# Kernel tuning notes

Hardware: AMD Instinct MI355X
Metric: run time of the kernel (lower is better)

Reference implementation:

```python
import jax, jax.numpy as jnp
import numpy as np

N, FDIM, HDIM, STEPS = 8192, 512, 1024, 50
STRESS, QNOISE = 0.0, 0.1


def setup_inputs() -> dict:
    key = jax.random.key(0)
    ks = jax.random.split(key, 20)
    s = 0.02
    d = {
        "real_antigen": jax.random.normal(ks[0], (N, FDIM), jnp.float32),
        "steps": STEPS,
        # quantum gene projection (self-loop graph -> per-node linear)
        "Wq": jax.random.normal(ks[1], (FDIM, HDIM), jnp.float32) * s,
        "bq": jnp.zeros((HDIM,), jnp.float32),
        # denoise_0: Linear(h,h) ReLU Linear(h,f)
        "W01": jax.random.normal(ks[2], (HDIM, HDIM), jnp.float32) * s,
        "b01": jnp.zeros((HDIM,), jnp.float32),
        "W02": jax.random.normal(ks[3], (HDIM, FDIM), jnp.float32) * s,
        "b02": jnp.zeros((FDIM,), jnp.float32),
        # denoise_1: Linear(h,h) Tanh Linear(h,f)
        "W11": jax.random.normal(ks[4], (HDIM, HDIM), jnp.float32) * s,
        "b11": jnp.zeros((HDIM,), jnp.float32),
        "W12": jax.random.normal(ks[5], (HDIM, FDIM), jnp.float32) * s,
        "b12": jnp.zeros((FDIM,), jnp.float32),
        # interference_net: Linear(2f,h) GELU Linear(h,f)
        "Wi1": jax.random.normal(ks[6], (2 * FDIM, HDIM), jnp.float32) * s,
        "bi1": jnp.zeros((HDIM,), jnp.float32),
        "Wi2": jax.random.normal(ks[7], (HDIM, FDIM), jnp.float32) * s,
        "bi2": jnp.zeros((FDIM,), jnp.float32),
        # quantum state scalars
        "alpha_amp": jnp.asarray(np.cos(0.6), jnp.float32),
        "beta_amp": jnp.asarray(np.sin(0.6), jnp.float32),
        "phase_cos": jnp.asarray(np.cos(0.3), jnp.float32),
    }
    return d


def reference(real_antigen, steps, Wq, bq, W01, b01, W02, b02, W11, b11,
              W12, b12, Wi1, bi1, Wi2, bi2, alpha_amp, beta_amp, phase_cos):
    sched = jnp.linspace(1e-4, 0.02, 100, dtype=jnp.float32)
    decoherence_rate = jnp.float32(0.1 + STRESS * 0.5)
    decay = jnp.exp(-decoherence_rate)
    # quantum probabilities (fixed amplitudes during the rollout)
    a2, b2 = alpha_amp ** 2, beta_amp ** 2
    p0 = a2 / (a2 + b2)
    p1 = b2 / (a2 + b2)
    sp0, sp1 = jnp.sqrt(p0), jnp.sqrt(p1)
    base_key = jax.random.key(1)
    x0 = jax.random.normal(jax.random.fold_in(base_key, 10_000), real_antigen.shape, jnp.float32)

    def step(carry, t):
        x, coh = carry
        qf = jax.nn.relu(x @ Wq + bq)                           # [N, H]
        d0 = jax.nn.relu(qf @ W01 + b01) @ W02 + b02            # [N, F]
        d1 = jnp.tanh(qf @ W11 + b11) @ W12 + b12               # [N, F]
        inter_in = jnp.concatenate([d0, d1], axis=-1)           # [N, 2F]
        interf = jax.nn.gelu(inter_in @ Wi1 + bi1, approximate=False) @ Wi2 + bi2
        qi = 2.0 * jnp.sqrt(p0 * p1) * phase_cos * coh          # scalar interference
        denoised = sp0 * d0 + sp1 * d1 + qi * interf
        alpha = jnp.maximum(1.0 - sched[t], 1e-8)
        alpha_prev = jnp.where(t > 0, 1.0 - sched[jnp.maximum(t - 1, 0)], 1.0)
        sqrt_1ma = jnp.sqrt(jnp.maximum(1.0 - alpha, 1e-8))
        x_new = (x - (1.0 - alpha) / sqrt_1ma * denoised) / jnp.sqrt(alpha)
        sigma = jnp.sqrt(jnp.maximum((1.0 - alpha_prev) / (1.0 - alpha) * (1.0 - alpha / alpha_prev), 0.0))
        noise = jax.random.normal(jax.random.fold_in(base_key, t), x.shape, jnp.float32)
        x_new = jnp.where(t > 0, x_new + (sigma + QNOISE * jnp.abs(qi)) * noise, x_new)
        return (x_new, coh * decay), None

    ts = jnp.arange(int(steps) - 1, -1, -1, dtype=jnp.int32)
    (x, _), _ = jax.lax.scan(step, (x0, jnp.float32(1.0)), ts)
    # quantum measurement: collapse to |0> with probability p0
    u = jax.random.uniform(jax.random.fold_in(base_key, 99_999), (), jnp.float32)
    dream = jnp.where(u < p0, 0.7 * x + 0.3 * real_antigen, x)
    return dream
```

## Files before the change

### kernel.cpp

```cpp
#include <hip/hip_runtime.h>
#include <stdint.h>
#include <math.h>


typedef __bf16 bf16x8 __attribute__((ext_vector_type(8)));
typedef float floatx4 __attribute__((ext_vector_type(4)));

__host__ __device__ inline void tf2x32(uint32_t k0, uint32_t k1,
                                       uint32_t x0, uint32_t x1,
                                       uint32_t& o0, uint32_t& o1) {
  uint32_t ks2 = k0 ^ k1 ^ 0x1BD11BDAu;
#define TF_R(r) { x0 += x1; x1 = (x1 << (r)) | (x1 >> (32 - (r))); x1 ^= x0; }
  x0 += k0; x1 += k1;
  TF_R(13) TF_R(15) TF_R(26) TF_R(6)
  x0 += k1;  x1 += ks2 + 1u;
  TF_R(17) TF_R(29) TF_R(16) TF_R(24)
  x0 += ks2; x1 += k0 + 2u;
  TF_R(13) TF_R(15) TF_R(26) TF_R(6)
  x0 += k0;  x1 += k1 + 3u;
  TF_R(17) TF_R(29) TF_R(16) TF_R(24)
  x0 += k1;  x1 += ks2 + 4u;
  TF_R(13) TF_R(15) TF_R(26) TF_R(6)
  x0 += ks2; x1 += k0 + 5u;
#undef TF_R
  o0 = x0; o1 = x1;
}

__device__ inline float erfinv_f32(float x) {
  float w = -log1pf(-x * x);
  float p;
  if (w < 5.0f) {
    w = w - 2.5f;
    p = 2.81022636e-08f;
    p = fmaf(p, w, 3.43273939e-07f);
    p = fmaf(p, w, -3.5233877e-06f);
    p = fmaf(p, w, -4.39150654e-06f);
    p = fmaf(p, w, 0.00021858087f);
    p = fmaf(p, w, -0.00125372503f);
    p = fmaf(p, w, -0.00417768164f);
    p = fmaf(p, w, 0.246640727f);
    p = fmaf(p, w, 1.50140941f);
  } else {
    w = sqrtf(w) - 3.0f;
    p = -0.000200214257f;
    p = fmaf(p, w, 0.000100950558f);
    p = fmaf(p, w, 0.00134934322f);
    p = fmaf(p, w, -0.00367342844f);
    p = fmaf(p, w, 0.00573950773f);
    p = fmaf(p, w, -0.0076224613f);
    p = fmaf(p, w, 0.00943887047f);
    p = fmaf(p, w, 1.00167406f);
    p = fmaf(p, w, 2.83297682f);
  }
  return p * x;
}

__device__ inline float tf_normal(uint32_t k0, uint32_t k1, uint32_t i) {
  uint32_t o0, o1;
  tf2x32(k0, k1, 0u, i, o0, o1);
  uint32_t bits = o0 ^ o1;
  float f = __uint_as_float(0x3F800000u | (bits >> 9)) - 1.0f;
  float u = f * 2.0f + (-0.99999994f);
  u = fmaxf(-0.99999994f, u);
  return 1.41421356f * erfinv_f32(u);
}

__device__ inline unsigned short f2bf(float f) {
  uint32_t u = __float_as_uint(f);
  u += 0x7FFFu + ((u >> 16) & 1u);
  return (unsigned short)(u >> 16);
}
__device__ inline float bf2f(unsigned short h) {
  return __uint_as_float(((uint32_t)h) << 16);
}

__global__ __launch_bounds__(256)
void transpose_bf16_kernel(const float* __restrict__ W,
                           unsigned short* __restrict__ Wt, int K, int N) {
  __shared__ float tile[32][33];
  int kb = blockIdx.x * 32, nb = blockIdx.y * 32;
  int tx = threadIdx.x & 31, ty = threadIdx.x >> 5;
#pragma unroll
  for (int i = 0; i < 32; i += 8)
    tile[ty + i][tx] = W[(size_t)(kb + ty + i) * N + nb + tx];
  __syncthreads();
#pragma unroll
  for (int i = 0; i < 32; i += 8)
    Wt[(size_t)(nb + ty + i) * K + kb + tx] = f2bf(tile[tx][ty + i]);
}

__device__ __forceinline__ void gemm_core_db(
    const unsigned short* __restrict__ A0, const unsigned short* __restrict__ A1,
    int lda0, int lda1, int K0, int Ktot,
    const unsigned short* __restrict__ Bt,
    int row0, int col0,
    unsigned short (*As)[128 * 32], unsigned short (*Bs)[128 * 32],
    floatx4 (&acc)[2][4]) {
  const int tid = threadIdx.x;
  const int wave = tid >> 6, lane = tid & 63;
  const int wr = wave >> 1, wc = wave & 1;
  const int srow = tid >> 2;
  const int sgr = (tid & 3) * 8;
  const int fm = lane & 15, quad = lane >> 4;

  auto issue = [&](int kt, int buf) {
    const int k0 = kt * 32;
    const unsigned short* Ap; int kOff, lda;
    if (k0 < K0) { Ap = A0; kOff = k0; lda = lda0; }
    else         { Ap = A1; kOff = k0 - K0; lda = lda1; }
    __builtin_amdgcn_global_load_lds(
        (const __attribute__((address_space(1))) uint32_t*)
            (Ap + (size_t)(row0 + srow) * lda + kOff + sgr),
        (__attribute__((address_space(3))) uint32_t*)(&As[buf][srow * 32 + sgr]),
        16, 0, 0);
    __builtin_amdgcn_global_load_lds(
        (const __attribute__((address_space(1))) uint32_t*)
            (Bt + (size_t)(col0 + srow) * Ktot + k0 + sgr),
        (__attribute__((address_space(3))) uint32_t*)(&Bs[buf][srow * 32 + sgr]),
        16, 0, 0);
  };

  const int nk = Ktot >> 5;
  issue(0, 0);
  for (int k = 0; k < nk; k++) {
    const int cur = k & 1;
    if (k + 1 < nk) {
      issue(k + 1, cur ^ 1);
      asm volatile("s_waitcnt vmcnt(2)\ns_barrier" ::: "memory");
    } else {
      asm volatile("s_waitcnt vmcnt(0)\ns_barrier" ::: "memory");
    }
    bf16x8 a[2], b[4];
#pragma unroll
    for (int tm = 0; tm < 2; tm++)
      a[tm] = *(const bf16x8*)(&As[cur][(wr * 32 + tm * 16 + fm) * 32 + quad * 8]);
#pragma unroll
    for (int tn = 0; tn < 4; tn++)
      b[tn] = *(const bf16x8*)(&Bs[cur][(wc * 64 + tn * 16 + fm) * 32 + quad * 8]);
#pragma unroll
    for (int tm = 0; tm < 2; tm++)
#pragma unroll
      for (int tn = 0; tn < 4; tn++)
        acc[tm][tn] = __builtin_amdgcn_mfma_f32_16x16x32_bf16(a[tm], b[tn],
                                                              acc[tm][tn], 0, 0, 0);
    asm volatile("s_barrier" ::: "memory");
  }
}

__device__ __forceinline__ void swizzled_block(int& row0, int& col0) {
  int id = blockIdx.x + gridDim.x * blockIdx.y;
  row0 = (id & 63) << 7;
  col0 = (id >> 6) << 7;
}

template<int ACT>
__global__ __launch_bounds__(512, 4)
void mfma_gemm(const unsigned short* __restrict__ A0,
               const unsigned short* __restrict__ A1,
               int lda0, int lda1, int K0, int Ktot,
               const unsigned short* __restrict__ Bt,
               const float* __restrict__ bias0,
               const float* __restrict__ bias1, int nsplit,
               unsigned short* __restrict__ C0,
               unsigned short* __restrict__ C1, int ldc) {
  __shared__ unsigned short As[2][128 * 32];
  __shared__ unsigned short Bs[2][128 * 32];
  int row0, col0;
  swizzled_block(row0, col0);
  floatx4 acc[2][4];
#pragma unroll
  for (int tm = 0; tm < 2; tm++)
#pragma unroll
    for (int tn = 0; tn < 4; tn++) acc[tm][tn] = (floatx4){0.f, 0.f, 0.f, 0.f};
  gemm_core_db(A0, A1, lda0, lda1, K0, Ktot, Bt, row0, col0, As, Bs, acc);

  const int lane = threadIdx.x & 63, wave = threadIdx.x >> 6;
  const int wr = wave >> 1, wc = wave & 1;
  const int fm = lane & 15, quad = lane >> 4;
  const bool side = (ACT == 4) && (col0 >= nsplit);
  const float* bias = side ? bias1 : bias0;
  unsigned short* C = side ? C1 : C0;
  const int cbase = col0 - (side ? nsplit : 0);
#pragma unroll
  for (int tn = 0; tn < 4; tn++) {
    int col = cbase + wc * 64 + tn * 16 + fm;
    float bv = bias[col];
#pragma unroll
    for (int tm = 0; tm < 2; tm++) {
      int rbase = row0 + wr * 32 + tm * 16 + quad * 4;
#pragma unroll
      for (int r = 0; r < 4; r++) {
        float val = acc[tm][tn][r] + bv;
        if (ACT == 1) val = fmaxf(val, 0.0f);
        if (ACT == 2) val = tanhf(val);
        if (ACT == 3) val = 0.5f * val * (1.0f + erff(val * 0.70710678118654752f));
        if (ACT == 4) val = side ? tanhf(val) : fmaxf(val, 0.0f);
        C[(size_t)(rbase + r) * ldc + col] = f2bf(val);
      }
    }
  }
}

__global__ __launch_bounds__(512, 4)
void mfma_gemm_pair(const unsigned short* __restrict__ Aa,
                    const unsigned short* __restrict__ Ab,
                    const unsigned short* __restrict__ Bta,
                    const unsigned short* __restrict__ Btb,
                    const float* __restrict__ biasa,
                    const float* __restrict__ biasb,
                    unsigned short* __restrict__ Ca,
                    unsigned short* __restrict__ Cb,
                    int Ktot, int ldc) {
  __shared__ unsigned short As[2][128 * 32];
  __shared__ unsigned short Bs[2][128 * 32];
  const int z = blockIdx.z;
  const unsigned short* A = z ? Ab : Aa;
  const unsigned short* Bt = z ? Btb : Bta;
  const float* bias = z ? biasb : biasa;
  unsigned short* C = z ? Cb : Ca;
  int row0, col0;
  swizzled_block(row0, col0);
  floatx4 acc[2][4];
#pragma unroll
  for (int tm = 0; tm < 2; tm++)
#pragma unroll
    for (int tn = 0; tn < 4; tn++) acc[tm][tn] = (floatx4){0.f, 0.f, 0.f, 0.f};
  gemm_core_db(A, A, Ktot, Ktot, Ktot, Ktot, Bt, row0, col0, As, Bs, acc);

  const int lane = threadIdx.x & 63, wave = threadIdx.x >> 6;
  const int wr = wave >> 1, wc = wave & 1;
  const int fm = lane & 15, quad = lane >> 4;
#pragma unroll
  for (int tn = 0; tn < 4; tn++) {
    int col = col0 + wc * 64 + tn * 16 + fm;
    float bv = bias[col];
#pragma unroll
    for (int tm = 0; tm < 2; tm++) {
      int rbase = row0 + wr * 32 + tm * 16 + quad * 4;
#pragma unroll
      for (int r = 0; r < 4; r++)
        C[(size_t)(rbase + r) * ldc + col] = f2bf(acc[tm][tn][r] + bv);
    }
  }
}

template<int MH, int NH>
__device__ __forceinline__ void phase_mfma8(bf16x8 (&a)[4][2], bf16x8 (&b)[4][2],
                                            floatx4 (&acc)[8][4]) {
  asm volatile("s_waitcnt lgkmcnt(0)" ::: "memory");
  __builtin_amdgcn_sched_barrier(0);
  __builtin_amdgcn_s_setprio(1);
#pragma unroll
  for (int s = 0; s < 2; s++)
#pragma unroll
    for (int mm = 0; mm < 4; mm++)
#pragma unroll
      for (int nn = 0; nn < 2; nn++)
        acc[MH * 4 + mm][NH * 2 + nn] = __builtin_amdgcn_mfma_f32_16x16x32_bf16(
            a[mm][s], b[NH * 2 + nn][s], acc[MH * 4 + mm][NH * 2 + nn], 0, 0, 0);
  __builtin_amdgcn_s_setprio(0);
}

__global__ __launch_bounds__(512, 2)
void mfma_gemm2_8ph(const unsigned short* __restrict__ A,
                    const unsigned short* __restrict__ Bt,
                    const float* __restrict__ bias0,
                    const float* __restrict__ bias1,
                    unsigned short* __restrict__ C0,
                    unsigned short* __restrict__ C1) {
  constexpr int NKT = 16;
  __shared__ unsigned short As[2][256 * 64];
  __shared__ unsigned short Bs[2][256 * 64];
  const int tid = threadIdx.x;
  const int wave = tid >> 6, lane = tid & 63;
  const int wr = wave >> 2, wc = wave & 3;
  const int fm = lane & 15, quad = lane >> 4;
  const int id = blockIdx.x;
  const int nid = (id & 7) * 32 + (id >> 3);
  const int row0 = (nid & 31) << 8;
  const int col0 = (nid >> 5) << 8;

  auto stageA = [&](int tile, int buf, int h) {
    if (tile >= NKT) return;
    const int kk = tile << 6;
#pragma unroll
    for (int c = 0; c < 2; c++) {
      int g2 = c * 512 + tid;
      int sr = g2 >> 3, gc = g2 & 7;
      __builtin_amdgcn_global_load_lds(
          (const __attribute__((address_space(1))) uint32_t*)
              (A + (size_t)(row0 + h * 128 + sr) * 1024 + kk + ((gc ^ (sr & 7)) << 3)),
          (__attribute__((address_space(3))) uint32_t*)(&As[buf][h * 8192 + g2 * 8]),
          16, 0, 0);
    }
  };
  auto stageB = [&](int tile, int buf, int h) {
    if (tile >= NKT) return;
    const int kk = tile << 6;
#pragma unroll
    for (int c = 0; c < 2; c++) {
      int g2 = c * 512 + tid;
      int sr = g2 >> 3, gc = g2 & 7;
      __builtin_amdgcn_global_load_lds(
          (const __attribute__((address_space(1))) uint32_t*)
              (Bt + (size_t)(col0 + h * 128 + sr) * 1024 + kk + ((gc ^ (sr & 7)) << 3)),
          (__attribute__((address_space(3))) uint32_t*)(&Bs[buf][h * 8192 + g2 * 8]),
          16, 0, 0);
    }
  };

  const int aswz = (fm & 7) << 3;
  auto rdA = [&](int buf, int m, int s) {
    return *(const bf16x8*)(&As[buf][(wr * 128 + m * 16 + fm) * 64 +
                                     ((s * 32 + quad * 8) ^ aswz)]);
  };
  auto rdB = [&](int buf, int n, int s) {
    return *(const bf16x8*)(&Bs[buf][(wc * 64 + n * 16 + fm) * 64 +
                                     ((s * 32 + quad * 8) ^ aswz)]);
  };

  floatx4 acc[8][4];
#pragma unroll
  for (int m = 0; m < 8; m++)
#pragma unroll
    for (int n = 0; n < 4; n++) acc[m][n] = (floatx4){0.f, 0.f, 0.f, 0.f};

  stageA(0, 0, 0); stageA(0, 0, 1);
  stageB(0, 0, 0); stageB(0, 0, 1);
  stageB(1, 1, 0); stageB(1, 1, 1);
  asm volatile("s_waitcnt vmcnt(4)" ::: "memory");
  asm volatile("s_barrier" ::: "memory");

#pragma unroll 1
  for (int j = 0; j < 8; j++) {
    const int t1 = 2 * j + 1;
    bf16x8 a[4][2], b[4][2];
#pragma unroll
    for (int mm = 0; mm < 4; mm++) { a[mm][0] = rdA(0, mm, 0); a[mm][1] = rdA(0, mm, 1); }
#pragma unroll
    for (int nn = 0; nn < 2; nn++) { b[nn][0] = rdB(0, nn, 0); b[nn][1] = rdB(0, nn, 1); }
    stageA(t1, 1, 0);
    asm volatile("s_barrier" ::: "memory");
    phase_mfma8<0, 0>(a, b, acc);
    asm volatile("s_barrier" ::: "memory");
#pragma unroll
    for (int nn = 2; nn < 4; nn++) { b[nn][0] = rdB(0, nn, 0); b[nn][1] = rdB(0, nn, 1); }
    stageA(t1, 1, 1);
    asm volatile("s_barrier" ::: "memory");
    phase_mfma8<0, 1>(a, b, acc);
    asm volatile("s_barrier" ::: "memory");
#pragma unroll
    for (int mm = 0; mm < 4; mm++) { a[mm][0] = rdA(0, 4 + mm, 0); a[mm][1] = rdA(0, 4 + mm, 1); }
    stageB(t1 + 1, 0, 0);
    asm volatile("s_barrier" ::: "memory");
    phase_mfma8<1, 1>(a, b, acc);
    asm volatile("s_barrier" ::: "memory");
    stageB(t1 + 1, 0, 1);
    asm volatile("s_barrier" ::: "memory");
    phase_mfma8<1, 0>(a, b, acc);
    if (j == 7) asm volatile("s_waitcnt vmcnt(0)" ::: "memory");
    else        asm volatile("s_waitcnt vmcnt(4)" ::: "memory");
    asm volatile("s_barrier" ::: "memory");
#pragma unroll
    for (int mm = 0; mm < 4; mm++) { a[mm][0] = rdA(1, mm, 0); a[mm][1] = rdA(1, mm, 1); }
#pragma unroll
    for (int nn = 0; nn < 2; nn++) { b[nn][0] = rdB(1, nn, 0); b[nn][1] = rdB(1, nn, 1); }
    stageA(t1 + 1, 0, 0);
    asm volatile("s_barrier" ::: "memory");
    phase_mfma8<0, 0>(a, b, acc);
    asm volatile("s_barrier" ::: "memory");
#pragma unroll
    for (int nn = 2; nn < 4; nn++) { b[nn][0] = rdB(1, nn, 0); b[nn][1] = rdB(1, nn, 1); }
    stageA(t1 + 1, 0, 1);
    asm volatile("s_barrier" ::: "memory");
    phase_mfma8<0, 1>(a, b, acc);
    asm volatile("s_barrier" ::: "memory");
#pragma unroll
    for (int mm = 0; mm < 4; mm++) { a[mm][0] = rdA(1, 4 + mm, 0); a[mm][1] = rdA(1, 4 + mm, 1); }
    stageB(t1 + 2, 1, 0);
    asm volatile("s_barrier" ::: "memory");
    phase_mfma8<1, 1>(a, b, acc);
    asm volatile("s_barrier" ::: "memory");
    stageB(t1 + 2, 1, 1);
    asm volatile("s_barrier" ::: "memory");
    phase_mfma8<1, 0>(a, b, acc);
    asm volatile("s_waitcnt vmcnt(4)" ::: "memory");
    asm volatile("s_barrier" ::: "memory");
  }

  const bool side = (col0 >= 1024);
  const float* bias = side ? bias1 : bias0;
  unsigned short* C = side ? C1 : C0;
  const int cb = col0 - (side ? 1024 : 0);
#pragma unroll
  for (int n = 0; n < 4; n++) {
    int col = cb + wc * 64 + n * 16 + fm;
    float bv = bias[col];
#pragma unroll
    for (int m = 0; m < 8; m++) {
      int rbase = row0 + wr * 128 + m * 16 + quad * 4;
#pragma unroll
      for (int r = 0; r < 4; r++) {
        float val = acc[m][n][r] + bv;
        val = side ? tanhf(val) : fmaxf(val, 0.0f);
        C[(size_t)(rbase + r) * 1024 + col] = f2bf(val);
      }
    }
  }
}

__global__ __launch_bounds__(512, 4)
void mfma_gemm_update(const unsigned short* __restrict__ A,
                      const unsigned short* __restrict__ Bt,
                      const float* __restrict__ bias,
                      const unsigned short* __restrict__ d0,
                      const unsigned short* __restrict__ d1,
                      float* __restrict__ x,
                      unsigned short* __restrict__ xbf,
                      const float* __restrict__ a_amp,
                      const float* __restrict__ b_amp,
                      const float* __restrict__ ph,
                      float coh, float c1, float sqa, float sigma,
                      int add_noise, uint32_t k0, uint32_t k1) {
  __shared__ unsigned short As[2][64 * 32];
  __shared__ unsigned short Bs[2][128 * 32];
  const int tid = threadIdx.x;
  const int wave = tid >> 6, lane = tid & 63;
  const int wr = wave >> 2, wc = wave & 3;
  const int fm = lane & 15, quad = lane >> 4;
  const int id = blockIdx.x + gridDim.x * blockIdx.y;
  const int row0 = (id & 127) << 6;
  const int col0 = (id >> 7) << 7;
  const int sArow = (tid & 255) >> 2;
  const int sBrow = tid >> 2;
  const int sgr = (tid & 3) * 8;

  auto issue = [&](int kt, int buf) {
    const int kk = kt * 32;
    __builtin_amdgcn_global_load_lds(
        (const __attribute__((address_space(1))) uint32_t*)
            (A + (size_t)(row0 + sArow) * 1024 + kk + sgr),
        (__attribute__((address_space(3))) uint32_t*)(&As[buf][sArow * 32 + sgr]),
        16, 0, 0);
    __builtin_amdgcn_global_load_lds(
        (const __attribute__((address_space(1))) uint32_t*)
            (Bt + (size_t)(col0 + sBrow) * 1024 + kk + sgr),
        (__attribute__((address_space(3))) uint32_t*)(&Bs[buf][sBrow * 32 + sgr]),
        16, 0, 0);
  };

  floatx4 acc[2][2];
#pragma unroll
  for (int tm = 0; tm < 2; tm++)
#pragma unroll
    for (int tn = 0; tn < 2; tn++) acc[tm][tn] = (floatx4){0.f, 0.f, 0.f, 0.f};

  const int nk = 32;
  issue(0, 0);
  for (int k = 0; k < nk; k++) {
    const int cur = k & 1;
    if (k + 1 < nk) {
      issue(k + 1, cur ^ 1);
      asm volatile("s_waitcnt vmcnt(2)\ns_barrier" ::: "memory");
    } else {
      asm volatile("s_waitcnt vmcnt(0)\ns_barrier" ::: "memory");
    }
    bf16x8 a[2], b[2];
#pragma unroll
    for (int tm = 0; tm < 2; tm++)
      a[tm] = *(const bf16x8*)(&As[cur][(wr * 32 + tm * 16 + fm) * 32 + quad * 8]);
#pragma unroll
    for (int tn = 0; tn < 2; tn++)
      b[tn] = *(const bf16x8*)(&Bs[cur][(wc * 32 + tn * 16 + fm) * 32 + quad * 8]);
#pragma unroll
    for (int tm = 0; tm < 2; tm++)
#pragma unroll
      for (int tn = 0; tn < 2; tn++)
        acc[tm][tn] = __builtin_amdgcn_mfma_f32_16x16x32_bf16(a[tm], b[tn],
                                                              acc[tm][tn], 0, 0, 0);
    asm volatile("s_barrier" ::: "memory");
  }

  float aa = a_amp[0], bb = b_amp[0], pc = ph[0];
  float a2 = aa * aa, b2 = bb * bb, s = a2 + b2;
  float p0 = a2 / s, p1 = b2 / s;
  float sp0 = sqrtf(p0), sp1 = sqrtf(p1);
  float qi = 2.0f * sqrtf(p0 * p1) * pc * coh;
  float nscale = sigma + 0.1f * fabsf(qi);

#pragma unroll
  for (int tn = 0; tn < 2; tn++) {
    int col = col0 + wc * 32 + tn * 16 + fm;
    float bv = bias[col];
#pragma unroll
    for (int tm = 0; tm < 2; tm++) {
      int rbase = row0 + wr * 32 + tm * 16 + quad * 4;
#pragma unroll
      for (int r = 0; r < 4; r++) {
        int row = rbase + r;
        size_t i = (size_t)row * 512 + col;
        float itf = acc[tm][tn][r] + bv;
        float den = sp0 * bf2f(d0[i]) + sp1 * bf2f(d1[i]) + qi * itf;
        float xn = (x[i] - c1 * den) / sqa;
        if (add_noise) xn += nscale * tf_normal(k0, k1, (uint32_t)i);
        x[i] = xn;
        xbf[i] = f2bf(xn);
      }
    }
  }
}

__global__ void init_normal_kernel(float* __restrict__ x,
                                   unsigned short* __restrict__ xbf,
                                   uint32_t k0, uint32_t k1, int n) {
  int i = blockIdx.x * blockDim.x + threadIdx.x;
  if (i >= n) return;
  float v = tf_normal(k0, k1, (uint32_t)i);
  x[i] = v;
  xbf[i] = f2bf(v);
}

__global__ void final_kernel(const float* __restrict__ x,
                             const float* __restrict__ real,
                             float* __restrict__ out,
                             const float* __restrict__ a_amp,
                             const float* __restrict__ b_amp,
                             uint32_t k0, uint32_t k1, int n) {
  int i = blockIdx.x * blockDim.x + threadIdx.x;
  if (i >= n) return;
  float aa = a_amp[0], bb = b_amp[0];
  float a2 = aa * aa, b2 = bb * bb;
  float p0 = a2 / (a2 + b2);
  uint32_t o0, o1;
  tf2x32(k0, k1, 0u, 0u, o0, o1);
  uint32_t bits = o0 ^ o1;
  float u = __uint_as_float(0x3F800000u | (bits >> 9)) - 1.0f;
  float xv = x[i];
  out[i] = (u < p0) ? (0.7f * xv + 0.3f * real[i]) : xv;
}

extern "C" void kernel_launch(void* const* d_in, const int* in_sizes, int n_in,
                              void* d_out, int out_size, void* d_ws,
                              size_t ws_size, hipStream_t stream) {
  const float* real = (const float*)d_in[0];
  const float* Wq  = (const float*)d_in[2];
  const float* bq  = (const float*)d_in[3];
  const float* W01 = (const float*)d_in[4];
  const float* b01 = (const float*)d_in[5];
  const float* W02 = (const float*)d_in[6];
  const float* b02 = (const float*)d_in[7];
  const float* W11 = (const float*)d_in[8];
  const float* b11 = (const float*)d_in[9];
  const float* W12 = (const float*)d_in[10];
  const float* b12 = (const float*)d_in[11];
  const float* Wi1 = (const float*)d_in[12];
  const float* bi1 = (const float*)d_in[13];
  const float* Wi2 = (const float*)d_in[14];
  const float* bi2 = (const float*)d_in[15];
  const float* a_amp = (const float*)d_in[16];
  const float* b_amp = (const float*)d_in[17];
  const float* ph    = (const float*)d_in[18];

  const int Nn = 8192, F = 512, H = 1024;
  const int nElem = Nn * F;
  const int NSPLIT_OFF = 1 << 30;

  char* ws = (char*)d_ws;
  float* x = (float*)ws;                                   ws += (size_t)nElem * 4;
  unsigned short* xbf = (unsigned short*)ws;               ws += (size_t)nElem * 2;
  unsigned short* qf  = (unsigned short*)ws;               ws += (size_t)Nn * H * 2;
  unsigned short* h0  = (unsigned short*)ws;               ws += (size_t)Nn * H * 2;
  unsigned short* h1  = (unsigned short*)ws;               ws += (size_t)Nn * H * 2;
  unsigned short* d0  = (unsigned short*)ws;               ws += (size_t)nElem * 2;
  unsigned short* d1  = (unsigned short*)ws;               ws += (size_t)nElem * 2;
  unsigned short* Wq_t  = (unsigned short*)ws;             ws += (size_t)F * H * 2;
  unsigned short* WA_t  = (unsigned short*)ws;             ws += (size_t)(2 * H) * H * 2;
  unsigned short* W02_t = (unsigned short*)ws;             ws += (size_t)H * F * 2;
  unsigned short* W12_t = (unsigned short*)ws;             ws += (size_t)H * F * 2;
  unsigned short* Wi1_t = (unsigned short*)ws;             ws += (size_t)(2 * F) * H * 2;
  unsigned short* Wi2_t = (unsigned short*)ws;             ws += (size_t)H * F * 2;

  dim3 tb(256);
  transpose_bf16_kernel<<<dim3(F / 32, H / 32), tb, 0, stream>>>(Wq, Wq_t, F, H);
  transpose_bf16_kernel<<<dim3(H / 32, H / 32), tb, 0, stream>>>(W01, WA_t, H, H);
  transpose_bf16_kernel<<<dim3(H / 32, H / 32), tb, 0, stream>>>(W11, WA_t + (size_t)H * H, H, H);
  transpose_bf16_kernel<<<dim3(H / 32, F / 32), tb, 0, stream>>>(W02, W02_t, H, F);
  transpose_bf16_kernel<<<dim3(H / 32, F / 32), tb, 0, stream>>>(W12, W12_t, H, F);
  transpose_bf16_kernel<<<dim3(2 * F / 32, H / 32), tb, 0, stream>>>(Wi1, Wi1_t, 2 * F, H);
  transpose_bf16_kernel<<<dim3(H / 32, F / 32), tb, 0, stream>>>(Wi2, Wi2_t, H, F);

  uint32_t kx0, kx1; tf2x32(0u, 1u, 0u, 10000u, kx0, kx1);
  init_normal_kernel<<<(nElem + 255) / 256, 256, 0, stream>>>(x, xbf, kx0, kx1, nElem);

  float sched[100];
  for (int i = 0; i < 100; i++)
    sched[i] = (float)(1e-4 + (0.02 - 1e-4) * (double)i / 99.0);
  const float decay = expf(-0.1f);
  float coh = 1.0f;

  dim3 blk(512);
  dim3 g1(H / 128, 64);
  dim3 g45(F / 128, 64, 2);
  dim3 g6(H / 128, 64);
  dim3 g7(F / 128, Nn / 64);

  for (int j = 0; j < 50; j++) {
    int t = 49 - j;
    mfma_gemm<1><<<g1, blk, 0, stream>>>(xbf, xbf, F, F, F, F, Wq_t,
                                         bq, nullptr, NSPLIT_OFF, qf, nullptr, H);
    mfma_gemm2_8ph<<<dim3(256), blk, 0, stream>>>(qf, WA_t, b01, b11, h0, h1);
    mfma_gemm_pair<<<g45, blk, 0, stream>>>(h0, h1, W02_t, W12_t, b02, b12,
                                            d0, d1, H, F);
    mfma_gemm<3><<<g6, blk, 0, stream>>>(d0, d1, F, F, F, 2 * F, Wi1_t,
                                         bi1, nullptr, NSPLIT_OFF, qf, nullptr, H);

    float schedt = sched[t];
    float alphaf = fmaxf(1.0f - schedt, 1e-8f);
    float one_m_alpha = 1.0f - alphaf;
    float sqrt_1ma = sqrtf(fmaxf(one_m_alpha, 1e-8f));
    float c1 = one_m_alpha / sqrt_1ma;
    float sqa = sqrtf(alphaf);
    float sigma = 0.0f;
    if (t > 0) {
      float ap = 1.0f - sched[t - 1];
      sigma = sqrtf(fmaxf((1.0f - ap) / one_m_alpha * (1.0f - alphaf / ap), 0.0f));
    }
    uint32_t kt0, kt1; tf2x32(0u, 1u, 0u, (uint32_t)t, kt0, kt1);
    mfma_gemm_update<<<g7, blk, 0, stream>>>(
        qf, Wi2_t, bi2, d0, d1, x, xbf, a_amp, b_amp, ph, coh, c1, sqa, sigma,
        (t > 0) ? 1 : 0, kt0, kt1);
    coh *= decay;
  }

  uint32_t ku0, ku1; tf2x32(0u, 1u, 0u, 99999u, ku0, ku1);
  final_kernel<<<(nElem + 255) / 256, 256, 0, stream>>>(
      x, real, (float*)d_out, a_amp, b_amp, ku0, ku1, nElem);
}
```

Baseline: 8.124 ms.

## Replace 128x128 double-buffered GEMMs with phased 128x256 swizzled-LDS kernel

```diff
diff --git a/kernel.cpp b/kernel.cpp
--- a/kernel.cpp
+++ b/kernel.cpp
@@ -89,161 +89,6 @@
     Wt[(size_t)(nb + ty + i) * K + kb + tx] = f2bf(tile[tx][ty + i]);
 }
 
-__device__ __forceinline__ void gemm_core_db(
-    const unsigned short* __restrict__ A0, const unsigned short* __restrict__ A1,
-    int lda0, int lda1, int K0, int Ktot,
-    const unsigned short* __restrict__ Bt,
-    int row0, int col0,
-    unsigned short (*As)[128 * 32], unsigned short (*Bs)[128 * 32],
-    floatx4 (&acc)[2][4]) {
-  const int tid = threadIdx.x;
-  const int wave = tid >> 6, lane = tid & 63;
-  const int wr = wave >> 1, wc = wave & 1;
-  const int srow = tid >> 2;
-  const int sgr = (tid & 3) * 8;
-  const int fm = lane & 15, quad = lane >> 4;
-
-  auto issue = [&](int kt, int buf) {
-    const int k0 = kt * 32;
-    const unsigned short* Ap; int kOff, lda;
-    if (k0 < K0) { Ap = A0; kOff = k0; lda = lda0; }
-    else         { Ap = A1; kOff = k0 - K0; lda = lda1; }
-    __builtin_amdgcn_global_load_lds(
-        (const __attribute__((address_space(1))) uint32_t*)
-            (Ap + (size_t)(row0 + srow) * lda + kOff + sgr),
-        (__attribute__((address_space(3))) uint32_t*)(&As[buf][srow * 32 + sgr]),
-        16, 0, 0);
-    __builtin_amdgcn_global_load_lds(
-        (const __attribute__((address_space(1))) uint32_t*)
-            (Bt + (size_t)(col0 + srow) * Ktot + k0 + sgr),
-        (__attribute__((address_space(3))) uint32_t*)(&Bs[buf][srow * 32 + sgr]),
-        16, 0, 0);
-  };
-
-  const int nk = Ktot >> 5;
-  issue(0, 0);
-  for (int k = 0; k < nk; k++) {
-    const int cur = k & 1;
-    if (k + 1 < nk) {
-      issue(k + 1, cur ^ 1);
-      asm volatile("s_waitcnt vmcnt(2)\ns_barrier" ::: "memory");
-    } else {
-      asm volatile("s_waitcnt vmcnt(0)\ns_barrier" ::: "memory");
-    }
-    bf16x8 a[2], b[4];
-#pragma unroll
-    for (int tm = 0; tm < 2; tm++)
-      a[tm] = *(const bf16x8*)(&As[cur][(wr * 32 + tm * 16 + fm) * 32 + quad * 8]);
-#pragma unroll
-    for (int tn = 0; tn < 4; tn++)
-      b[tn] = *(const bf16x8*)(&Bs[cur][(wc * 64 + tn * 16 + fm) * 32 + quad * 8]);
-#pragma unroll
-    for (int tm = 0; tm < 2; tm++)
-#pragma unroll
-      for (int tn = 0; tn < 4; tn++)
-        acc[tm][tn] = __builtin_amdgcn_mfma_f32_16x16x32_bf16(a[tm], b[tn],
-                                                              acc[tm][tn], 0, 0, 0);
-    asm volatile("s_barrier" ::: "memory");
-  }
-}
-
-__device__ __forceinline__ void swizzled_block(int& row0, int& col0) {
-  int id = blockIdx.x + gridDim.x * blockIdx.y;
-  row0 = (id & 63) << 7;
-  col0 = (id >> 6) << 7;
-}
-
-template<int ACT>
-__global__ __launch_bounds__(512, 4)
-void mfma_gemm(const unsigned short* __restrict__ A0,
-               const unsigned short* __restrict__ A1,
-               int lda0, int lda1, int K0, int Ktot,
-               const unsigned short* __restrict__ Bt,
-               const float* __restrict__ bias0,
-               const float* __restrict__ bias1, int nsplit,
-               unsigned short* __restrict__ C0,
-               unsigned short* __restrict__ C1, int ldc) {
-  __shared__ unsigned short As[2][128 * 32];
-  __shared__ unsigned short Bs[2][128 * 32];
-  int row0, col0;
-  swizzled_block(row0, col0);
-  floatx4 acc[2][4];
-#pragma unroll
-  for (int tm = 0; tm < 2; tm++)
-#pragma unroll
-    for (int tn = 0; tn < 4; tn++) acc[tm][tn] = (floatx4){0.f, 0.f, 0.f, 0.f};
-  gemm_core_db(A0, A1, lda0, lda1, K0, Ktot, Bt, row0, col0, As, Bs, acc);
-
-  const int lane = threadIdx.x & 63, wave = threadIdx.x >> 6;
-  const int wr = wave >> 1, wc = wave & 1;
-  const int fm = lane & 15, quad = lane >> 4;
-  const bool side = (ACT == 4) && (col0 >= nsplit);
-  const float* bias = side ? bias1 : bias0;
-  unsigned short* C = side ? C1 : C0;
-  const int cbase = col0 - (side ? nsplit : 0);
-#pragma unroll
-  for (int tn = 0; tn < 4; tn++) {
-    int col = cbase + wc * 64 + tn * 16 + fm;
-    float bv = bias[col];
-#pragma unroll
-    for (int tm = 0; tm < 2; tm++) {
-      int rbase = row0 + wr * 32 + tm * 16 + quad * 4;
-#pragma unroll
-      for (int r = 0; r < 4; r++) {
-        float val = acc[tm][tn][r] + bv;
-        if (ACT == 1) val = fmaxf(val, 0.0f);
-        if (ACT == 2) val = tanhf(val);
-        if (ACT == 3) val = 0.5f * val * (1.0f + erff(val * 0.70710678118654752f));
-        if (ACT == 4) val = side ? tanhf(val) : fmaxf(val, 0.0f);
-        C[(size_t)(rbase + r) * ldc + col] = f2bf(val);
-      }
-    }
-  }
-}
-
-__global__ __launch_bounds__(512, 4)
-void mfma_gemm_pair(const unsigned short* __restrict__ Aa,
-                    const unsigned short* __restrict__ Ab,
-                    const unsigned short* __restrict__ Bta,
-                    const unsigned short* __restrict__ Btb,
-                    const float* __restrict__ biasa,
-                    const float* __restrict__ biasb,
-                    unsigned short* __restrict__ Ca,
-                    unsigned short* __restrict__ Cb,
-                    int Ktot, int ldc) {
-  __shared__ unsigned short As[2][128 * 32];
-  __shared__ unsigned short Bs[2][128 * 32];
-  const int z = blockIdx.z;
-  const unsigned short* A = z ? Ab : Aa;
-  const unsigned short* Bt = z ? Btb : Bta;
-  const float* bias = z ? biasb : biasa;
-  unsigned short* C = z ? Cb : Ca;
-  int row0, col0;
-  swizzled_block(row0, col0);
-  floatx4 acc[2][4];
-#pragma unroll
-  for (int tm = 0; tm < 2; tm++)
-#pragma unroll
-    for (int tn = 0; tn < 4; tn++) acc[tm][tn] = (floatx4){0.f, 0.f, 0.f, 0.f};
-  gemm_core_db(A, A, Ktot, Ktot, Ktot, Ktot, Bt, row0, col0, As, Bs, acc);
-
-  const int lane = threadIdx.x & 63, wave = threadIdx.x >> 6;
-  const int wr = wave >> 1, wc = wave & 1;
-  const int fm = lane & 15, quad = lane >> 4;
-#pragma unroll
-  for (int tn = 0; tn < 4; tn++) {
-    int col = col0 + wc * 64 + tn * 16 + fm;
-    float bv = bias[col];
-#pragma unroll
-    for (int tm = 0; tm < 2; tm++) {
-      int rbase = row0 + wr * 32 + tm * 16 + quad * 4;
-#pragma unroll
-      for (int r = 0; r < 4; r++)
-        C[(size_t)(rbase + r) * ldc + col] = f2bf(acc[tm][tn][r] + bv);
-    }
-  }
-}
-
 template<int MH, int NH>
 __device__ __forceinline__ void phase_mfma8(bf16x8 (&a)[4][2], bf16x8 (&b)[4][2],
                                             floatx4 (&acc)[8][4]) {
@@ -259,6 +104,182 @@
         acc[MH * 4 + mm][NH * 2 + nn] = __builtin_amdgcn_mfma_f32_16x16x32_bf16(
             a[mm][s], b[NH * 2 + nn][s], acc[MH * 4 + mm][NH * 2 + nn], 0, 0, 0);
   __builtin_amdgcn_s_setprio(0);
+}
+
+template<int MH, int NH>
+__device__ __forceinline__ void phase_mfma4(bf16x8 (&a)[4][2], bf16x8 (&b)[4][2],
+                                            floatx4 (&acc)[4][4]) {
+  asm volatile("s_waitcnt lgkmcnt(0)" ::: "memory");
+  __builtin_amdgcn_sched_barrier(0);
+  __builtin_amdgcn_s_setprio(1);
+#pragma unroll
+  for (int s = 0; s < 2; s++)
+#pragma unroll
+    for (int mm = 0; mm < 2; mm++)
+#pragma unroll
+      for (int nn = 0; nn < 2; nn++)
+        acc[MH * 2 + mm][NH * 2 + nn] = __builtin_amdgcn_mfma_f32_16x16x32_bf16(
+            a[MH * 2 + mm][s], b[NH * 2 + nn][s], acc[MH * 2 + mm][NH * 2 + nn],
+            0, 0, 0);
+  __builtin_amdgcn_s_setprio(0);
+}
+
+template<int ACT, int PAIR>
+__global__ __launch_bounds__(512, 2)
+void mfma_gemm_8ph_128x256(const unsigned short* __restrict__ A0,
+                           const unsigned short* __restrict__ A1,
+                           int lda0, int lda1, int K0, int Ktot,
+                           const unsigned short* __restrict__ Bt,
+                           const float* __restrict__ bias,
+                           unsigned short* __restrict__ C, int ldc,
+                           const unsigned short* __restrict__ Ab,
+                           const unsigned short* __restrict__ Btb,
+                           const float* __restrict__ biasb,
+                           unsigned short* __restrict__ Cb) {
+  __shared__ unsigned short As[2][128 * 64];
+  __shared__ unsigned short Bs[2][256 * 64];
+  const int tid = threadIdx.x;
+  const int wave = tid >> 6, lane = tid & 63;
+  const int wr = wave >> 2, wc = wave & 3;
+  const int fm = lane & 15, quad = lane >> 4;
+  const int id = blockIdx.x;
+  const int nid = (id & 7) * 32 + (id >> 3);
+  int row0, col0;
+  if (PAIR) {
+    const int rem = nid & 127;
+    row0 = (rem & 63) << 7;
+    col0 = (rem >> 6) << 8;
+    if (nid >> 7) { A0 = Ab; A1 = Ab; Bt = Btb; bias = biasb; C = Cb; }
+  } else {
+    row0 = (nid & 63) << 7;
+    col0 = (nid >> 6) << 8;
+  }
+  const int NKT = Ktot >> 6;
+
+  auto stageA = [&](int tile, int buf, int h) {
+    if (tile >= NKT) return;
+    const int kk = tile << 6;
+    const unsigned short* Ap; int kOff, lda;
+    if (kk < K0) { Ap = A0; kOff = kk; lda = lda0; }
+    else         { Ap = A1; kOff = kk - K0; lda = lda1; }
+    const int sr = tid >> 3, gc = tid & 7;
+    __builtin_amdgcn_global_load_lds(
+        (const __attribute__((address_space(1))) uint32_t*)
+            (Ap + (size_t)(row0 + h * 64 + sr) * lda + kOff + ((gc ^ (sr & 7)) << 3)),
+        (__attribute__((address_space(3))) uint32_t*)(&As[buf][h * 4096 + tid * 8]),
+        16, 0, 0);
+  };
+  auto stageB = [&](int tile, int buf, int h) {
+    if (tile >= NKT) return;
+    const int kk = tile << 6;
+#pragma unroll
+    for (int c = 0; c < 2; c++) {
+      int g2 = c * 512 + tid;
+      int sr = g2 >> 3, gc = g2 & 7;
+      __builtin_amdgcn_global_load_lds(
+          (const __attribute__((address_space(1))) uint32_t*)
+              (Bt + (size_t)(col0 + h * 128 + sr) * Ktot + kk + ((gc ^ (sr & 7)) << 3)),
+          (__attribute__((address_space(3))) uint32_t*)(&Bs[buf][h * 8192 + g2 * 8]),
+          16, 0, 0);
+    }
+  };
+
+  const int aswz = (fm & 7) << 3;
+  auto rdA = [&](int buf, int m, int s) {
+    return *(const bf16x8*)(&As[buf][(wr * 64 + m * 16 + fm) * 64 +
+                                     ((s * 32 + quad * 8) ^ aswz)]);
+  };
+  auto rdB = [&](int buf, int n, int s) {
+    return *(const bf16x8*)(&Bs[buf][(wc * 64 + n * 16 + fm) * 64 +
+                                     ((s * 32 + quad * 8) ^ aswz)]);
+  };
+
+  floatx4 acc[4][4];
+#pragma unroll
+  for (int m = 0; m < 4; m++)
+#pragma unroll
+    for (int n = 0; n < 4; n++) acc[m][n] = (floatx4){0.f, 0.f, 0.f, 0.f};
+
+  stageA(0, 0, 0); stageA(0, 0, 1);
+  stageB(0, 0, 0); stageB(0, 0, 1);
+  stageB(1, 1, 0); stageB(1, 1, 1);
+  asm volatile("s_waitcnt vmcnt(4)" ::: "memory");
+  asm volatile("s_barrier" ::: "memory");
+
+  const int NJ = NKT >> 1;
+#pragma unroll 1
+  for (int j = 0; j < NJ; j++) {
+    const int t1 = 2 * j + 1;
+    bf16x8 a[4][2], b[4][2];
+#pragma unroll
+    for (int mm = 0; mm < 2; mm++) { a[mm][0] = rdA(0, mm, 0); a[mm][1] = rdA(0, mm, 1); }
+#pragma unroll
+    for (int nn = 0; nn < 2; nn++) { b[nn][0] = rdB(0, nn, 0); b[nn][1] = rdB(0, nn, 1); }
+    stageA(t1, 1, 0);
+    asm volatile("s_barrier" ::: "memory");
+    phase_mfma4<0, 0>(a, b, acc);
+    asm volatile("s_barrier" ::: "memory");
+#pragma unroll
+    for (int nn = 2; nn < 4; nn++) { b[nn][0] = rdB(0, nn, 0); b[nn][1] = rdB(0, nn, 1); }
+    stageA(t1, 1, 1);
+    asm volatile("s_barrier" ::: "memory");
+    phase_mfma4<0, 1>(a, b, acc);
+    asm volatile("s_barrier" ::: "memory");
+#pragma unroll
+    for (int mm = 2; mm < 4; mm++) { a[mm][0] = rdA(0, mm, 0); a[mm][1] = rdA(0, mm, 1); }
+    stageB(t1 + 1, 0, 0);
+    asm volatile("s_barrier" ::: "memory");
+    phase_mfma4<1, 1>(a, b, acc);
+    asm volatile("s_barrier" ::: "memory");
+    stageB(t1 + 1, 0, 1);
+    asm volatile("s_barrier" ::: "memory");
+    phase_mfma4<1, 0>(a, b, acc);
+    if (j == NJ - 1) asm volatile("s_waitcnt vmcnt(0)" ::: "memory");
+    else             asm volatile("s_waitcnt vmcnt(4)" ::: "memory");
+    asm volatile("s_barrier" ::: "memory");
+#pragma unroll
+    for (int mm = 0; mm < 2; mm++) { a[mm][0] = rdA(1, mm, 0); a[mm][1] = rdA(1, mm, 1); }
+#pragma unroll
+    for (int nn = 0; nn < 2; nn++) { b[nn][0] = rdB(1, nn, 0); b[nn][1] = rdB(1, nn, 1); }
+    stageA(t1 + 1, 0, 0);
+    asm volatile("s_barrier" ::: "memory");
+    phase_mfma4<0, 0>(a, b, acc);
+    asm volatile("s_barrier" ::: "memory");
+#pragma unroll
+    for (int nn = 2; nn < 4; nn++) { b[nn][0] = rdB(1, nn, 0); b[nn][1] = rdB(1, nn, 1); }
+    stageA(t1 + 1, 0, 1);
+    asm volatile("s_barrier" ::: "memory");
+    phase_mfma4<0, 1>(a, b, acc);
+    asm volatile("s_barrier" ::: "memory");
+#pragma unroll
+    for (int mm = 2; mm < 4; mm++) { a[mm][0] = rdA(1, mm, 0); a[mm][1] = rdA(1, mm, 1); }
+    stageB(t1 + 2, 1, 0);
+    asm volatile("s_barrier" ::: "memory");
+    phase_mfma4<1, 1>(a, b, acc);
+    asm volatile("s_barrier" ::: "memory");
+    stageB(t1 + 2, 1, 1);
+    asm volatile("s_barrier" ::: "memory");
+    phase_mfma4<1, 0>(a, b, acc);
+    asm volatile("s_waitcnt vmcnt(4)" ::: "memory");
+    asm volatile("s_barrier" ::: "memory");
+  }
+
+#pragma unroll
+  for (int n = 0; n < 4; n++) {
+    int col = col0 + wc * 64 + n * 16 + fm;
+    float bv = bias[col];
+#pragma unroll
+    for (int m = 0; m < 4; m++) {
+      int rbase = row0 + wr * 64 + m * 16 + quad * 4;
+#pragma unroll
+      for (int r = 0; r < 4; r++) {
+        float val = acc[m][n][r] + bv;
+        if (ACT == 1) val = fmaxf(val, 0.0f);
+        if (ACT == 3) val = 0.5f * val * (1.0f + erff(val * 0.70710678118654752f));
+        C[(size_t)(rbase + r) * ldc + col] = f2bf(val);
+      }
+    }
+  }
 }
 
 __global__ __launch_bounds__(512, 2)
@@ -563,7 +584,6 @@
 
   const int Nn = 8192, F = 512, H = 1024;
   const int nElem = Nn * F;
-  const int NSPLIT_OFF = 1 << 30;
 
   char* ws = (char*)d_ws;
   float* x = (float*)ws;                                   ws += (size_t)nElem * 4;
@@ -599,20 +619,21 @@
   float coh = 1.0f;
 
   dim3 blk(512);
-  dim3 g1(H / 128, 64);
-  dim3 g45(F / 128, 64, 2);
-  dim3 g6(H / 128, 64);
+  dim3 g8(256);
   dim3 g7(F / 128, Nn / 64);
 
   for (int j = 0; j < 50; j++) {
     int t = 49 - j;
-    mfma_gemm<1><<<g1, blk, 0, stream>>>(xbf, xbf, F, F, F, F, Wq_t,
-                                         bq, nullptr, NSPLIT_OFF, qf, nullptr, H);
-    mfma_gemm2_8ph<<<dim3(256), blk, 0, stream>>>(qf, WA_t, b01, b11, h0, h1);
-    mfma_gemm_pair<<<g45, blk, 0, stream>>>(h0, h1, W02_t, W12_t, b02, b12,
-                                            d0, d1, H, F);
-    mfma_gemm<3><<<g6, blk, 0, stream>>>(d0, d1, F, F, F, 2 * F, Wi1_t,
-                                         bi1, nullptr, NSPLIT_OFF, qf, nullptr, H);
+    mfma_gemm_8ph_128x256<1, 0><<<g8, blk, 0, stream>>>(
+        xbf, xbf, F, F, F, F, Wq_t, bq, qf, H,
+        nullptr, nullptr, nullptr, nullptr);
+    mfma_gemm2_8ph<<<g8, blk, 0, stream>>>(qf, WA_t, b01, b11, h0, h1);
+    mfma_gemm_8ph_128x256<0, 1><<<g8, blk, 0, stream>>>(
+        h0, h0, H, H, H, H, W02_t, b02, d0, F,
+        h1, W12_t, b12, d1);
+    mfma_gemm_8ph_128x256<3, 0><<<g8, blk, 0, stream>>>(
+        d0, d1, F, F, F, 2 * F, Wi1_t, bi1, qf, H,
+        nullptr, nullptr, nullptr, nullptr);
 
     float schedt = sched[t];
     float alphaf = fmaxf(1.0f - schedt, 1e-8f);
```

Result: no change. 8.053 ms, median of 3 (-0.9%).
